# Performance work log

Hardware: AMD Instinct MI355X
Metric: run time of the kernel (lower is better)

## Reference

```python
import jax, jax.numpy as jnp
import numpy as np
from jax import lax

B, T, D, H, L = 2048, 512, 64, 16, 10
LOG2PI = float(np.log(2.0 * np.pi))


def _gru_cell(x, h, Wih, Whh, bih, bhh):
    # torch GRUCell gate order: r, z, n
    gi = x @ Wih.T + bih
    gh = h @ Whh.T + bhh
    ir, iz, inn = jnp.split(gi, 3, axis=-1)
    hr, hz, hn = jnp.split(gh, 3, axis=-1)
    r = jax.nn.sigmoid(ir + hr)
    z = jax.nn.sigmoid(iz + hz)
    n = jnp.tanh(inn + r * hn)
    return (1.0 - z) * n + z * h


def _mlp_head(h, W1, b1, W2, b2, Wmu, bmu, Wcov, bcov):
    hh = jax.nn.relu(h @ W1.T + b1)
    hh = jax.nn.relu(hh @ W2.T + b2)
    mu = hh @ Wmu.T + bmu
    sigma = jnp.exp(hh @ Wcov.T + bcov)
    return mu, sigma


def setup_inputs():
    key = jax.random.key(0)
    ks = jax.random.split(key, 24)

    def he(k, shape, fan_in):
        return jax.random.normal(k, shape, dtype=jnp.float32) * np.float32(np.sqrt(2.0 / fan_in))

    z = lambda *s: jnp.zeros(s, jnp.float32)
    p = {}
    p['x'] = jax.random.normal(ks[0], (B, T, D), dtype=jnp.float32)
    p['eps'] = jax.random.normal(ks[1], (B, T, L), dtype=jnp.float32)
    # bidirectional inference GRU
    p['bi_Wih_f'] = he(ks[2], (3 * H, D), D); p['bi_Whh_f'] = he(ks[3], (3 * H, H), H)
    p['bi_bih_f'] = z(3 * H); p['bi_bhh_f'] = z(3 * H)
    p['bi_Wih_b'] = he(ks[4], (3 * H, D), D); p['bi_Whh_b'] = he(ks[5], (3 * H, H), H)
    p['bi_bih_b'] = z(3 * H); p['bi_bhh_b'] = z(3 * H)
    # inference GRUCell on [z_prev, context]
    p['infz_Wih'] = he(ks[6], (3 * H, L + 2 * H), L + 2 * H); p['infz_Whh'] = he(ks[7], (3 * H, H), H)
    p['infz_bih'] = z(3 * H); p['infz_bhh'] = z(3 * H)
    # inference MLP
    p['inf_W1'] = he(ks[8], (H, H), H); p['inf_b1'] = z(H)
    p['inf_W2'] = he(ks[9], (H, H), H); p['inf_b2'] = z(H)
    p['inf_Wmu'] = he(ks[10], (L, H), H); p['inf_bmu'] = z(L)
    p['inf_Wcov'] = he(ks[11], (L, H), H); p['inf_bcov'] = z(L)
    # generative prior GRUCell + MLP (frozen in torch)
    p['genz_Wih'] = he(ks[12], (3 * H, L), L); p['genz_Whh'] = he(ks[13], (3 * H, H), H)
    p['genz_bih'] = z(3 * H); p['genz_bhh'] = z(3 * H)
    p['genzmlp_W1'] = he(ks[14], (H, H), H); p['genzmlp_b1'] = z(H)
    p['genzmlp_W2'] = he(ks[15], (H, H), H); p['genzmlp_b2'] = z(H)
    p['genzmlp_Wmu'] = he(ks[16], (L, H), H); p['genzmlp_bmu'] = z(L)
    p['genzmlp_Wcov'] = he(ks[17], (L, H), H); p['genzmlp_bcov'] = z(L)
    # generative emission GRUCell + MLP (outputs 3*D)
    p['genr_Wih'] = he(ks[18], (3 * H, L), L); p['genr_Whh'] = he(ks[19], (3 * H, H), H)
    p['genr_bih'] = z(3 * H); p['genr_bhh'] = z(3 * H)
    p['genr_W1'] = he(ks[20], (H, H), H); p['genr_b1'] = z(H)
    p['genr_W2'] = he(ks[21], (3 * D, H), H); p['genr_b2'] = z(3 * D)
    return p


def _forward(x, eps, bi_Wih_f, bi_Whh_f, bi_bih_f, bi_bhh_f, bi_Wih_b, bi_Whh_b, bi_bih_b, bi_bhh_b,
             infz_Wih, infz_Whh, infz_bih, infz_bhh,
             inf_W1, inf_b1, inf_W2, inf_b2, inf_Wmu, inf_bmu, inf_Wcov, inf_bcov,
             genz_Wih, genz_Whh, genz_bih, genz_bhh,
             genzmlp_W1, genzmlp_b1, genzmlp_W2, genzmlp_b2, genzmlp_Wmu, genzmlp_bmu, genzmlp_Wcov, genzmlp_bcov,
             genr_Wih, genr_Whh, genr_bih, genr_bhh, genr_W1, genr_b1, genr_W2, genr_b2):
    b, t, d = x.shape
    xt = jnp.transpose(x, (1, 0, 2))      # [T, B, D] time-major
    eps_t = jnp.transpose(eps, (1, 0, 2))  # [T, B, L]
    h0 = jnp.zeros((b, H), x.dtype)

    def fstep(h, xin):
        h2 = _gru_cell(xin, h, bi_Wih_f, bi_Whh_f, bi_bih_f, bi_bhh_f)
        return h2, h2

    def bstep(h, xin):
        h2 = _gru_cell(xin, h, bi_Wih_b, bi_Whh_b, bi_bih_b, bi_bhh_b)
        return h2, h2

    _, fwd = lax.scan(fstep, h0, xt)               # [T, B, H]
    _, bwd_rev = lax.scan(bstep, h0, xt[::-1])
    bwd = bwd_rev[::-1]                            # [T, B, H]

    pad = jnp.zeros((1, b, H), x.dtype)
    h_right = jnp.concatenate([pad, fwd[:-1]], axis=0)   # h^{->}_{t-1}
    h_left = jnp.concatenate([bwd[1:], pad], axis=0)     # h^{<-}_{t+1}
    ctx = jnp.concatenate([h_right, h_left], axis=-1)    # [T, B, 2H]

    def step(carry, inp):
        h_z, h_gz, h_gr, z_prev = carry
        c, e, xi = inp
        h_z = _gru_cell(jnp.concatenate([z_prev, c], axis=-1), h_z, infz_Wih, infz_Whh, infz_bih, infz_bhh)
        q_mu, q_sig = _mlp_head(h_z, inf_W1, inf_b1, inf_W2, inf_b2, inf_Wmu, inf_bmu, inf_Wcov, inf_bcov)
        h_gz = _gru_cell(z_prev, h_gz, genz_Wih, genz_Whh, genz_bih, genz_bhh)
        p_mu, p_sig = _mlp_head(h_gz, genzmlp_W1, genzmlp_b1, genzmlp_W2, genzmlp_b2, genzmlp_Wmu, genzmlp_bmu, genzmlp_Wcov, genzmlp_bcov)
        # KL(N(q_mu,q_sig) || N(p_mu,p_sig))
        kl = jnp.log(p_sig / q_sig) + (q_sig * q_sig + (q_mu - p_mu) ** 2) / (2.0 * p_sig * p_sig) - 0.5
        kl_t = kl.sum(axis=-1).mean()
        z_t = q_mu + q_sig * e  # rsample
        h_gr = _gru_cell(z_t, h_gr, genr_Wih, genr_Whh, genr_bih, genr_bhh)
        r = jax.nn.relu(h_gr @ genr_W1.T + genr_b1) @ genr_W2.T + genr_b2  # [B, 3D]
        r_mu = r[:, :d]
        r_diag = jnp.exp(r[:, d:2 * d]) + 1e-4
        w = r[:, 2 * d:]  # rank-1 cov factor
        # LowRankMVN log_prob via Woodbury (rank 1): Cov = D + w w^T
        delta = xi - r_mu
        dinv = 1.0 / r_diag
        wd = w * dinv
        cap = 1.0 + jnp.sum(wd * w, axis=-1)  # capacitance
        maha = jnp.sum(delta * delta * dinv, axis=-1) - jnp.sum(wd * delta, axis=-1) ** 2 / cap
        logdet = jnp.sum(jnp.log(r_diag), axis=-1) + jnp.log(cap)
        logp = -0.5 * (d * LOG2PI + logdet + maha)
        nll_t = -logp.mean()
        return (h_z, h_gz, h_gr, z_t), (kl_t, nll_t)

    z0 = jnp.zeros((b, L), x.dtype)
    carry0 = (h0, h0, h0, z0)
    _, (kls, nlls) = lax.scan(step, carry0, (ctx, eps_t, xt))
    return nlls.sum(), kls.sum()


def reference(x, eps, bi_Wih_f, bi_Whh_f, bi_bih_f, bi_bhh_f, bi_Wih_b, bi_Whh_b, bi_bih_b, bi_bhh_b,
              infz_Wih, infz_Whh, infz_bih, infz_bhh,
              inf_W1, inf_b1, inf_W2, inf_b2, inf_Wmu, inf_bmu, inf_Wcov, inf_bcov,
              genz_Wih, genz_Whh, genz_bih, genz_bhh,
              genzmlp_W1, genzmlp_b1, genzmlp_W2, genzmlp_b2, genzmlp_Wmu, genzmlp_bmu, genzmlp_Wcov, genzmlp_bcov,
              genr_Wih, genr_Whh, genr_bih, genr_bhh, genr_W1, genr_b1, genr_W2, genr_b2):
    return _forward(x, eps, bi_Wih_f, bi_Whh_f, bi_bih_f, bi_bhh_f, bi_Wih_b, bi_Whh_b, bi_bih_b, bi_bhh_b,
                    infz_Wih, infz_Whh, infz_bih, infz_bhh,
                    inf_W1, inf_b1, inf_W2, inf_b2, inf_Wmu, inf_bmu, inf_Wcov, inf_bcov,
                    genz_Wih, genz_Whh, genz_bih, genz_bhh,
                    genzmlp_W1, genzmlp_b1, genzmlp_W2, genzmlp_b2, genzmlp_Wmu, genzmlp_bmu, genzmlp_Wcov, genzmlp_bcov,
                    genr_Wih, genr_Whh, genr_bih, genr_bhh, genr_W1, genr_b1, genr_W2, genr_b2)
```

## Files before the change

kernel.cpp:

```cpp
#include <hip/hip_runtime.h>

namespace {

typedef __attribute__((ext_vector_type(4))) _Float16 half4v;
typedef __attribute__((ext_vector_type(4))) float   float4v;
typedef unsigned int u32;

#define MFMA16(a,b,c) __builtin_amdgcn_mfma_f32_16x16x16f16((a),(b),(c),0,0,0)

constexpr int Bb = 2048;
constexpr int Tt = 512;
constexpr float LOG2PI_ = 1.8378770664093453f;

struct InPtrs { const float* p[42]; };

__device__ __forceinline__ float rcpf(float x){ return __builtin_amdgcn_rcpf(x); }
__device__ __forceinline__ float sigm(float x){ return rcpf(1.0f + __expf(-x)); }
__device__ __forceinline__ float tanh_(float x){ return 1.0f - 2.0f*rcpf(1.0f + __expf(2.0f*x)); }

__device__ __forceinline__ void barrier_lds(){
  asm volatile("s_waitcnt lgkmcnt(0)" ::: "memory");
  __builtin_amdgcn_s_barrier();
  asm volatile("" ::: "memory");
}

__global__ void zero2(float* out){ if (threadIdx.x < 2) out[threadIdx.x] = 0.f; }

__device__ __forceinline__ void gru_update(const float4v& Dr, const float4v& Dz,
                                           const float4v& Dn, const float4v& Dh, half4v& hB){
  #pragma unroll
  for (int i = 0; i < 4; ++i){
    const float rr = sigm(Dr[i]);
    const float zz = sigm(Dz[i]);
    const float nn = tanh_(Dn[i] + rr*Dh[i]);
    const float hp = (float)hB[i];
    hB[i] = (_Float16)(nn + zz*(hp - nn));
  }
}

__device__ __forceinline__ half4v relu_pack(const float4v& D){
  half4v o;
  #pragma unroll
  for (int i = 0; i < 4; ++i) o[i] = (_Float16)fmaxf(D[i], 0.f);
  return o;
}

constexpr int CH = 8;
constexpr int NCH = Tt / CH;

__global__ __launch_bounds__(128,1) void bigru(InPtrs ip, _Float16* __restrict__ hf,
                                               _Float16* __restrict__ hb)
{
  const int tid = threadIdx.x;
  const int w = tid >> 6;
  const int l = tid & 63, r = l & 15, q = l >> 4;
  const int dir = blockIdx.y;
  const int base = blockIdx.x * 16;

  const float* __restrict__ x   = ip.p[0];
  const float* __restrict__ Wih = dir ? ip.p[6] : ip.p[2];
  const float* __restrict__ Whh = dir ? ip.p[7] : ip.p[3];
  const float* __restrict__ bih = dir ? ip.p[8] : ip.p[4];
  const float* __restrict__ bhh = dir ? ip.p[9] : ip.p[5];
  _Float16* __restrict__ hout = dir ? hb : hf;

  __shared__ __align__(16) float giS[2][CH][64][12];

  half4v Wi[3][4];
  float  b0[4], b1[4], b2[4];
  float4v xp[CH][4];
  half4v Wh[3];
  float  bh2[4];
  half4v hB = {0,0,0,0};
  const float* xrow = x + (size_t)(base + r) * Tt * 64;

  if (w == 1){
    #pragma unroll
    for (int rt = 0; rt < 3; ++rt)
      #pragma unroll
      for (int kt = 0; kt < 4; ++kt)
        #pragma unroll
        for (int j = 0; j < 4; ++j)
          Wi[rt][kt][j] = (_Float16)Wih[(rt*16 + r)*64 + kt*16 + q*4 + j];
    #pragma unroll
    for (int i = 0; i < 4; ++i){
      const int row = q*4 + i;
      b0[i] = bih[row]      + bhh[row];
      b1[i] = bih[16 + row] + bhh[16 + row];
      b2[i] = bih[32 + row];
    }
    #pragma unroll
    for (int s = 0; s < CH; ++s){
      const int tn = dir ? Tt-1-s : s;
      #pragma unroll
      for (int kt = 0; kt < 4; ++kt)
        xp[s][kt] = *(const float4v*)(xrow + (size_t)tn*64 + kt*16 + q*4);
    }
  } else {
    #pragma unroll
    for (int rt = 0; rt < 3; ++rt)
      #pragma unroll
      for (int j = 0; j < 4; ++j)
        Wh[rt][j] = (_Float16)Whh[(rt*16 + r)*16 + q*4 + j];
    #pragma unroll
    for (int i = 0; i < 4; ++i) bh2[i] = bhh[32 + q*4 + i];
  }

  for (int c = 0; c < NCH; ++c){
    if (w == 1){
      #pragma unroll
      for (int st = 0; st < CH; ++st){
        const int tg = c*CH + st;
        half4v xB[4];
        #pragma unroll
        for (int kt = 0; kt < 4; ++kt)
          #pragma unroll
          for (int j = 0; j < 4; ++j) xB[kt][j] = (_Float16)xp[st][kt][j];
        const int tp = tg + CH;
        if (tp < Tt){
          const int tn = dir ? Tt-1-tp : tp;
          #pragma unroll
          for (int kt = 0; kt < 4; ++kt)
            xp[st][kt] = *(const float4v*)(xrow + (size_t)tn*64 + kt*16 + q*4);
        }
        float4v A0 = {b0[0],b0[1],b0[2],b0[3]};
        float4v A1 = {b1[0],b1[1],b1[2],b1[3]};
        float4v A2 = {b2[0],b2[1],b2[2],b2[3]};
        #pragma unroll
        for (int kt = 0; kt < 4; ++kt){
          A0 = MFMA16(Wi[0][kt], xB[kt], A0);
          A1 = MFMA16(Wi[1][kt], xB[kt], A1);
          A2 = MFMA16(Wi[2][kt], xB[kt], A2);
        }
        float* o = &giS[c&1][st][l][0];
        *(float4v*)(o + 0) = A0;
        *(float4v*)(o + 4) = A1;
        *(float4v*)(o + 8) = A2;
      }
    }
    barrier_lds();
    if (w == 0){
      #pragma unroll
      for (int st = 0; st < CH; ++st){
        const int tg = c*CH + st;
        const int t = dir ? Tt-1-tg : tg;
        const float* gi = &giS[c&1][st][l][0];
        float4v A0 = *(const float4v*)(gi + 0);
        float4v A1 = *(const float4v*)(gi + 4);
        float4v A2 = *(const float4v*)(gi + 8);
        float4v Dh = {bh2[0],bh2[1],bh2[2],bh2[3]};
        A0 = MFMA16(Wh[0], hB, A0);
        A1 = MFMA16(Wh[1], hB, A1);
        Dh = MFMA16(Wh[2], hB, Dh);
        gru_update(A0, A1, A2, Dh, hB);
        *(half4v*)(hout + (((size_t)t*Bb + base + r) << 4) + q*4) = hB;
      }
    }
  }
}

__global__ __launch_bounds__(192,1) void vae_seq(InPtrs ip, const _Float16* __restrict__ hf,
                                                 const _Float16* __restrict__ hb,
                                                 _Float16* __restrict__ hz,
                                                 _Float16* __restrict__ hgz,
                                                 _Float16* __restrict__ hgr)
{
  const int tid = threadIdx.x;
  const int w = tid / 64;
  const int l = tid & 63, r = l & 15, q = l >> 4;
  const int base = blockIdx.x * 16;
  const int row0 = q*4;

  __shared__ u32 zS[3][2][64];
  for (int i = tid; i < 3*2*64; i += 192) ((u32*)zS)[i] = 0u;
  barrier_lds();

  half4v WizA[3][3], WhzA[3], I1A, I2A, IMuA, ICovA;
  float bz0[4], bz1[4], bzn[4], bzh[4], bI1v[4], bI2v[4], bIMu[4], bICov[4];
  half4v hzB = {0,0,0,0}, zB = {0,0,0,0};
  half4v hrR[4], hlR[4];
  float4v eR[4];
  half4v WgzA[3], WhgzA[3];
  float bg0[4], bg1[4], bgn[4], bgh[4];
  half4v hgzB = {0,0,0,0};
  half4v WgrA[3], WhgrA[3];
  float br0[4], br1[4], brn[4], brh[4];
  half4v hgrB = {0,0,0,0};

  const float* erow = ip.p[1] + (size_t)(base + r) * Tt * 10;

  if (w == 0){
    #pragma unroll
    for (int rt = 0; rt < 3; ++rt)
      #pragma unroll
      for (int kt = 0; kt < 3; ++kt)
        #pragma unroll
        for (int j = 0; j < 4; ++j){
          const int k = kt*16 + q*4 + j;
          int c;
          if (kt == 0) c = (k < 10) ? k : -1;
          else if (kt == 1) c = 10 + (k - 16);
          else c = 26 + (k - 32);
          WizA[rt][kt][j] = (c >= 0) ? (_Float16)ip.p[10][(rt*16 + r)*42 + c] : (_Float16)0.f;
        }
    #pragma unroll
    for (int rt = 0; rt < 3; ++rt)
      #pragma unroll
      for (int j = 0; j < 4; ++j)
        WhzA[rt][j] = (_Float16)ip.p[11][(rt*16 + r)*16 + q*4 + j];
    #pragma unroll
    for (int j = 0; j < 4; ++j){
      const int k = q*4 + j;
      I1A[j]  = (_Float16)ip.p[14][r*16 + k];
      I2A[j]  = (_Float16)ip.p[16][r*16 + k];
      IMuA[j] = (r < 10) ? (_Float16)ip.p[18][r*16 + k] : (_Float16)0.f;
      ICovA[j]= (r < 10) ? (_Float16)ip.p[20][r*16 + k] : (_Float16)0.f;
    }
    #pragma unroll
    for (int i = 0; i < 4; ++i){
      const int row = row0 + i;
      bz0[i] = ip.p[12][row]    + ip.p[13][row];
      bz1[i] = ip.p[12][16+row] + ip.p[13][16+row];
      bzn[i] = ip.p[12][32+row];
      bzh[i] = ip.p[13][32+row];
      bI1v[i] = ip.p[15][row];  bI2v[i] = ip.p[17][row];
      bIMu[i]  = (row < 10) ? ip.p[19][row] : 0.f;
      bICov[i] = (row < 10) ? ip.p[21][row] : 0.f;
    }
    #pragma unroll
    for (int s = 0; s < 4; ++s){
      if (s >= 1) hrR[s] = *(const half4v*)(hf + (((size_t)(s-1)*Bb + base + r) << 4) + q*4);
      else { half4v z0 = {0,0,0,0}; hrR[s] = z0; }
      hlR[s] = *(const half4v*)(hb + (((size_t)(s+1)*Bb + base + r) << 4) + q*4);
      float4v et;
      #pragma unroll
      for (int ii = 0; ii < 4; ++ii) et[ii] = (row0 + ii < 10) ? erow[s*10 + row0 + ii] : 0.f;
      eR[s] = et;
    }
  } else if (w == 1){
    #pragma unroll
    for (int rt = 0; rt < 3; ++rt)
      #pragma unroll
      for (int j = 0; j < 4; ++j){
        const int k = q*4 + j;
        WgzA[rt][j]  = (k < 10) ? (_Float16)ip.p[22][(rt*16 + r)*10 + k] : (_Float16)0.f;
        WhgzA[rt][j] = (_Float16)ip.p[23][(rt*16 + r)*16 + k];
      }
    #pragma unroll
    for (int i = 0; i < 4; ++i){
      const int row = row0 + i;
      bg0[i] = ip.p[24][row]    + ip.p[25][row];
      bg1[i] = ip.p[24][16+row] + ip.p[25][16+row];
      bgn[i] = ip.p[24][32+row];
      bgh[i] = ip.p[25][32+row];
    }
  } else {
    #pragma unroll
    for (int rt = 0; rt < 3; ++rt)
      #pragma unroll
      for (int j = 0; j < 4; ++j){
        const int k = q*4 + j;
        WgrA[rt][j]  = (k < 10) ? (_Float16)ip.p[34][(rt*16 + r)*10 + k] : (_Float16)0.f;
        WhgrA[rt][j] = (_Float16)ip.p[35][(rt*16 + r)*16 + k];
      }
    #pragma unroll
    for (int i = 0; i < 4; ++i){
      const int row = row0 + i;
      br0[i] = ip.p[36][row]    + ip.p[37][row];
      br1[i] = ip.p[36][16+row] + ip.p[37][16+row];
      brn[i] = ip.p[36][32+row];
      brh[i] = ip.p[37][32+row];
    }
  }

  for (int ib = 0; ib < Tt + 4; ib += 4){
    #pragma unroll
    for (int k = 0; k < 4; ++k){
      const int i = ib + k;
      if (w == 0){
        if (i < Tt){
          const half4v hrB = hrR[k], hlB = hlR[k];
          const float4v ev = eR[k];
          const int f = i + 4;
          if (f < Tt){
            hrR[k] = *(const half4v*)(hf + (((size_t)(f-1)*Bb + base + r) << 4) + q*4);
            if (f <= Tt-2) hlR[k] = *(const half4v*)(hb + (((size_t)(f+1)*Bb + base + r) << 4) + q*4);
            else { half4v z0 = {0,0,0,0}; hlR[k] = z0; }
            float4v et;
            #pragma unroll
            for (int ii = 0; ii < 4; ++ii) et[ii] = (row0 + ii < 10) ? erow[f*10 + row0 + ii] : 0.f;
            eR[k] = et;
          }
          float4v Dr = {bz0[0],bz0[1],bz0[2],bz0[3]};
          float4v Dz = {bz1[0],bz1[1],bz1[2],bz1[3]};
          float4v Dn = {bzn[0],bzn[1],bzn[2],bzn[3]};
          float4v Dh = {bzh[0],bzh[1],bzh[2],bzh[3]};
          Dr = MFMA16(WizA[0][1], hrB, Dr); Dr = MFMA16(WizA[0][2], hlB, Dr);
          Dz = MFMA16(WizA[1][1], hrB, Dz); Dz = MFMA16(WizA[1][2], hlB, Dz);
          Dn = MFMA16(WizA[2][1], hrB, Dn); Dn = MFMA16(WizA[2][2], hlB, Dn);
          Dr = MFMA16(WhzA[0], hzB, Dr);
          Dz = MFMA16(WhzA[1], hzB, Dz);
          Dh = MFMA16(WhzA[2], hzB, Dh);
          Dr = MFMA16(WizA[0][0], zB, Dr);
          Dz = MFMA16(WizA[1][0], zB, Dz);
          Dn = MFMA16(WizA[2][0], zB, Dn);
          gru_update(Dr, Dz, Dn, Dh, hzB);
          *(half4v*)(hz + (((size_t)i*Bb + base + r) << 4) + q*4) = hzB;

          float4v H1 = {bI1v[0],bI1v[1],bI1v[2],bI1v[3]};
          H1 = MFMA16(I1A, hzB, H1);
          const half4v h1B = relu_pack(H1);
          float4v H2 = {bI2v[0],bI2v[1],bI2v[2],bI2v[3]};
          H2 = MFMA16(I2A, h1B, H2);
          const half4v h2B = relu_pack(H2);
          float4v Qmu  = {bIMu[0],bIMu[1],bIMu[2],bIMu[3]};
          float4v Qpre = {bICov[0],bICov[1],bICov[2],bICov[3]};
          Qmu  = MFMA16(IMuA,  h2B, Qmu);
          Qpre = MFMA16(ICovA, h2B, Qpre);

          const int slot = i % 3;
          #pragma unroll
          for (int ii = 0; ii < 4; ++ii){
            const float qs = __expf(Qpre[ii]);
            zB[ii] = (_Float16)(Qmu[ii] + qs*ev[ii]);
          }
          union { half4v h; u32 u[2]; } zc; zc.h = zB;
          zS[slot][0][l] = zc.u[0];
          zS[slot][1][l] = zc.u[1];
        }
      } else if (w == 1){
        if (i >= 1 && i <= Tt){
          const int s = i - 1;
          const int sp = (s - 1 + 3) % 3;
          union { half4v h; u32 u[2]; } zc;
          zc.u[0] = zS[sp][0][l]; zc.u[1] = zS[sp][1][l];
          const half4v zPrev = zc.h;

          float4v Er = {bg0[0],bg0[1],bg0[2],bg0[3]};
          float4v Ez = {bg1[0],bg1[1],bg1[2],bg1[3]};
          float4v En = {bgn[0],bgn[1],bgn[2],bgn[3]};
          float4v Eh = {bgh[0],bgh[1],bgh[2],bgh[3]};
          Er = MFMA16(WgzA[0], zPrev, Er); Er = MFMA16(WhgzA[0], hgzB, Er);
          Ez = MFMA16(WgzA[1], zPrev, Ez); Ez = MFMA16(WhgzA[1], hgzB, Ez);
          En = MFMA16(WgzA[2], zPrev, En);
          Eh = MFMA16(WhgzA[2], hgzB, Eh);
          gru_update(Er, Ez, En, Eh, hgzB);
          *(half4v*)(hgz + (((size_t)s*Bb + base + r) << 4) + q*4) = hgzB;
        }
      } else {
        if (i >= 2 && i < Tt + 2){
          const int u = i - 2;
          union { half4v h; u32 uu[2]; } zc;
          zc.uu[0] = zS[u % 3][0][l]; zc.uu[1] = zS[u % 3][1][l];
          const half4v zU = zc.h;

          float4v Fr = {br0[0],br0[1],br0[2],br0[3]};
          float4v Fz = {br1[0],br1[1],br1[2],br1[3]};
          float4v Fn = {brn[0],brn[1],brn[2],brn[3]};
          float4v Fh = {brh[0],brh[1],brh[2],brh[3]};
          Fr = MFMA16(WgrA[0], zU, Fr); Fr = MFMA16(WhgrA[0], hgrB, Fr);
          Fz = MFMA16(WgrA[1], zU, Fz); Fz = MFMA16(WhgrA[1], hgrB, Fz);
          Fn = MFMA16(WgrA[2], zU, Fn);
          Fh = MFMA16(WhgrA[2], hgrB, Fh);
          gru_update(Fr, Fz, Fn, Fh, hgrB);
          *(half4v*)(hgr + (((size_t)u*Bb + base + r) << 4) + q*4) = hgrB;
        }
      }
      barrier_lds();
    }
  }
}

__global__ __launch_bounds__(256,2) void epi(InPtrs ip, const _Float16* __restrict__ hz,
                                             const _Float16* __restrict__ hgz,
                                             const _Float16* __restrict__ hgr,
                                             float* __restrict__ out)
{
  const int tid = threadIdx.x;
  const int l = tid & 63, r = l & 15, q = l >> 4;
  const int row0 = q*4;

  if (blockIdx.x < 1024){
    const int wid = blockIdx.x * 4 + (tid >> 6);
    const int u0 = wid * 16;

    half4v I1A, I2A, IMuA, ICovA, Z1A, Z2A, ZMuA, ZCovA;
    float bI1v[4], bI2v[4], bIMu[4], bICov[4], bZ1v[4], bZ2v[4], bZMu[4], bZCov[4];
    #pragma unroll
    for (int j = 0; j < 4; ++j){
      const int k = q*4 + j;
      I1A[j]  = (_Float16)ip.p[14][r*16 + k];
      I2A[j]  = (_Float16)ip.p[16][r*16 + k];
      IMuA[j] = (r < 10) ? (_Float16)ip.p[18][r*16 + k] : (_Float16)0.f;
      ICovA[j]= (r < 10) ? (_Float16)ip.p[20][r*16 + k] : (_Float16)0.f;
      Z1A[j]  = (_Float16)ip.p[26][r*16 + k];
      Z2A[j]  = (_Float16)ip.p[28][r*16 + k];
      ZMuA[j] = (r < 10) ? (_Float16)ip.p[30][r*16 + k] : (_Float16)0.f;
      ZCovA[j]= (r < 10) ? (_Float16)ip.p[32][r*16 + k] : (_Float16)0.f;
    }
    #pragma unroll
    for (int i = 0; i < 4; ++i){
      const int row = row0 + i;
      bI1v[i] = ip.p[15][row];  bI2v[i] = ip.p[17][row];
      bIMu[i]  = (row < 10) ? ip.p[19][row] : 0.f;
      bICov[i] = (row < 10) ? ip.p[21][row] : 0.f;
      bZ1v[i] = ip.p[27][row];  bZ2v[i] = ip.p[29][row];
      bZMu[i]  = (row < 10) ? ip.p[31][row] : 0.f;
      bZCov[i] = (row < 10) ? ip.p[33][row] : 0.f;
    }

    float kl_acc = 0.f;
    for (int k = 0; k < 16; ++k){
      const int u = u0 + k;
      const int tile = u >> 9, t = u & 511;
      const size_t off = (((size_t)t*Bb + tile*16 + r) << 4) + q*4;
      const half4v hzB  = *(const half4v*)(hz  + off);
      const half4v hgzB = *(const half4v*)(hgz + off);

      float4v H1 = {bI1v[0],bI1v[1],bI1v[2],bI1v[3]};
      H1 = MFMA16(I1A, hzB, H1);
      const half4v h1B = relu_pack(H1);
      float4v H2 = {bI2v[0],bI2v[1],bI2v[2],bI2v[3]};
      H2 = MFMA16(I2A, h1B, H2);
      const half4v h2B = relu_pack(H2);
      float4v Qmu  = {bIMu[0],bIMu[1],bIMu[2],bIMu[3]};
      float4v Qpre = {bICov[0],bICov[1],bICov[2],bICov[3]};
      Qmu  = MFMA16(IMuA,  h2B, Qmu);
      Qpre = MFMA16(ICovA, h2B, Qpre);

      float4v G1 = {bZ1v[0],bZ1v[1],bZ1v[2],bZ1v[3]};
      G1 = MFMA16(Z1A, hgzB, G1);
      const half4v g1B = relu_pack(G1);
      float4v G2 = {bZ2v[0],bZ2v[1],bZ2v[2],bZ2v[3]};
      G2 = MFMA16(Z2A, g1B, G2);
      const half4v g2B = relu_pack(G2);
      float4v Pmu  = {bZMu[0],bZMu[1],bZMu[2],bZMu[3]};
      float4v Ppre = {bZCov[0],bZCov[1],bZCov[2],bZCov[3]};
      Pmu  = MFMA16(ZMuA,  g2B, Pmu);
      Ppre = MFMA16(ZCovA, g2B, Ppre);

      #pragma unroll
      for (int ii = 0; ii < 4; ++ii){
        const float qs = __expf(Qpre[ii]);
        const float dm = Qmu[ii] - Pmu[ii];
        kl_acc += (Ppre[ii] - Qpre[ii]) + (qs*qs + dm*dm)*0.5f*__expf(-2.f*Ppre[ii]) - 0.5f;
      }
    }
    #pragma unroll
    for (int m = 1; m < 64; m <<= 1) kl_acc += __shfl_xor(kl_acc, m, 64);
    if (l == 0) atomicAdd(&out[1], kl_acc * (1.f/(float)Bb));
  } else {
    const int wid = (blockIdx.x - 1024) * 4 + (tid >> 6);
    const int u0 = wid * 16;

    half4v R1A, R2A[12];
    float bR1v[4], bR2v[12][4];
    #pragma unroll
    for (int j = 0; j < 4; ++j){
      const int k = q*4 + j;
      R1A[j] = (_Float16)ip.p[38][r*16 + k];
      #pragma unroll
      for (int m = 0; m < 12; ++m)
        R2A[m][j] = (_Float16)ip.p[40][(m*16 + r)*16 + k];
    }
    #pragma unroll
    for (int i = 0; i < 4; ++i){
      const int row = row0 + i;
      bR1v[i] = ip.p[39][row];
      #pragma unroll
      for (int m = 0; m < 12; ++m) bR2v[m][i] = ip.p[41][m*16 + row];
    }

    float nll_acc = 0.f;
    for (int k = 0; k < 16; ++k){
      const int u = u0 + k;
      const int tile = u >> 9, t = u & 511;
      const half4v hgrB = *(const half4v*)(hgr + (((size_t)t*Bb + tile*16 + r) << 4) + q*4);
      const float* xrow = ip.p[0] + ((size_t)(tile*16 + r) * Tt + t) * 64;
      float4v xv[4];
      #pragma unroll
      for (int m = 0; m < 4; ++m) xv[m] = *(const float4v*)(xrow + m*16 + q*4);

      float4v R1D = {bR1v[0],bR1v[1],bR1v[2],bR1v[3]};
      R1D = MFMA16(R1A, hgrB, R1D);
      const half4v r1B = relu_pack(R1D);

      float s1 = 0.f, s2 = 0.f, s3 = 0.f, s4 = 0.f;
      #pragma unroll
      for (int m = 0; m < 4; ++m){
        float4v Dmu = {bR2v[m][0],bR2v[m][1],bR2v[m][2],bR2v[m][3]};
        float4v Ddp = {bR2v[4+m][0],bR2v[4+m][1],bR2v[4+m][2],bR2v[4+m][3]};
        float4v Dw  = {bR2v[8+m][0],bR2v[8+m][1],bR2v[8+m][2],bR2v[8+m][3]};
        Dmu = MFMA16(R2A[m],   r1B, Dmu);
        Ddp = MFMA16(R2A[4+m], r1B, Ddp);
        Dw  = MFMA16(R2A[8+m], r1B, Dw);
        #pragma unroll
        for (int ii = 0; ii < 4; ++ii){
          const float diag = __expf(Ddp[ii]) + 1e-4f;
          const float dinv = rcpf(diag);
          const float delta = xv[m][ii] - Dmu[ii];
          const float wv = Dw[ii];
          s1 += delta*delta*dinv;
          s2 += wv*wv*dinv;
          s3 += wv*dinv*delta;
          s4 += __logf(diag);
        }
      }
      s1 += __shfl_xor(s1, 16, 64); s1 += __shfl_xor(s1, 32, 64);
      s2 += __shfl_xor(s2, 16, 64); s2 += __shfl_xor(s2, 32, 64);
      s3 += __shfl_xor(s3, 16, 64); s3 += __shfl_xor(s3, 32, 64);
      s4 += __shfl_xor(s4, 16, 64); s4 += __shfl_xor(s4, 32, 64);
      const float cap = 1.f + s2;
      const float maha = s1 - s3*s3*rcpf(cap);
      const float logdet = s4 + __logf(cap);
      nll_acc += 0.5f*(64.f*LOG2PI_ + logdet + maha);
    }
    #pragma unroll
    for (int m = 1; m < 64; m <<= 1) nll_acc += __shfl_xor(nll_acc, m, 64);
    if (l == 0) atomicAdd(&out[0], nll_acc * 0.25f * (1.f/(float)Bb));
  }
}

}

extern "C" void kernel_launch(void* const* d_in, const int* in_sizes, int n_in,
                              void* d_out, int out_size, void* d_ws, size_t ws_size,
                              hipStream_t stream)
{
  InPtrs ip;
  for (int i = 0; i < 42; ++i) ip.p[i] = (const float*)d_in[i];
  float* out = (float*)d_out;

  const size_t SZ = (size_t)Tt * Bb * 16;
  _Float16* hf  = (_Float16*)d_ws;
  _Float16* hb  = hf  + SZ;
  _Float16* hz  = hb  + SZ;
  _Float16* hgz = hz  + SZ;
  _Float16* hgr = hgz + SZ;

  zero2<<<1, 64, 0, stream>>>(out);
  dim3 gb(Bb/16, 2);
  bigru<<<gb, 128, 0, stream>>>(ip, hf, hb);
  vae_seq<<<Bb/16, 192, 0, stream>>>(ip, hf, hb, hz, hgz, hgr);
  epi<<<2048, 256, 0, stream>>>(ip, hz, hgz, hgr, out);
}
```

Before: 1.029 ms.

## Split input projection across two warps, halve barriers, widen epilogue grid, fold zeroing

The bidirectional GRU now uses two producer waves that each compute input-gate projections for alternating timesteps, which halves per-wave work and prefetch registers. The zeroing of the outputs moves into the bigru kernel, removing one launch. In the sequential VAE kernel the z ring buffer grows from 3 to 8 slots, the pipeline stage offsets are widened, and the block barrier fires only every other step. The epilogue launches twice as many blocks with half the work per wave. The barrier skipping depends on the deeper ring and the larger lag being sufficient to avoid races, and zeroing inside bigru assumes it happens before any epilogue atomics, which stream ordering provides.

Measured after the change: 1.135 ms. 1.1x slower.

```diff
diff --git a/kernel.cpp b/kernel.cpp
--- a/kernel.cpp
+++ b/kernel.cpp
@@ -23,8 +23,6 @@
   __builtin_amdgcn_s_barrier();
   asm volatile("" ::: "memory");
 }
-
-__global__ void zero2(float* out){ if (threadIdx.x < 2) out[threadIdx.x] = 0.f; }
 
 __device__ __forceinline__ void gru_update(const float4v& Dr, const float4v& Dz,
                                            const float4v& Dn, const float4v& Dh, half4v& hB){
@@ -48,14 +46,16 @@
 constexpr int CH = 8;
 constexpr int NCH = Tt / CH;
 
-__global__ __launch_bounds__(128,1) void bigru(InPtrs ip, _Float16* __restrict__ hf,
-                                               _Float16* __restrict__ hb)
+__global__ __launch_bounds__(192,1) void bigru(InPtrs ip, _Float16* __restrict__ hf,
+                                               _Float16* __restrict__ hb, float* __restrict__ out)
 {
   const int tid = threadIdx.x;
-  const int w = tid >> 6;
+  const int w = tid / 64;
   const int l = tid & 63, r = l & 15, q = l >> 4;
   const int dir = blockIdx.y;
   const int base = blockIdx.x * 16;
+
+  if (blockIdx.x == 0 && blockIdx.y == 0 && tid < 2) out[tid] = 0.f;
 
   const float* __restrict__ x   = ip.p[0];
   const float* __restrict__ Wih = dir ? ip.p[6] : ip.p[2];
@@ -68,13 +68,14 @@
 
   half4v Wi[3][4];
   float  b0[4], b1[4], b2[4];
-  float4v xp[CH][4];
+  float4v xp[4][4];
   half4v Wh[3];
   float  bh2[4];
   half4v hB = {0,0,0,0};
   const float* xrow = x + (size_t)(base + r) * Tt * 64;
-
-  if (w == 1){
+  const int p = w - 1;
+
+  if (w >= 1){
     #pragma unroll
     for (int rt = 0; rt < 3; ++rt)
       #pragma unroll
@@ -90,11 +91,12 @@
       b2[i] = bih[32 + row];
     }
     #pragma unroll
-    for (int s = 0; s < CH; ++s){
-      const int tn = dir ? Tt-1-s : s;
+    for (int sl = 0; sl < 4; ++sl){
+      const int tg = sl*2 + p;
+      const int tn = dir ? Tt-1-tg : tg;
       #pragma unroll
       for (int kt = 0; kt < 4; ++kt)
-        xp[s][kt] = *(const float4v*)(xrow + (size_t)tn*64 + kt*16 + q*4);
+        xp[sl][kt] = *(const float4v*)(xrow + (size_t)tn*64 + kt*16 + q*4);
     }
   } else {
     #pragma unroll
@@ -107,21 +109,22 @@
   }
 
   for (int c = 0; c < NCH; ++c){
-    if (w == 1){
-      #pragma unroll
-      for (int st = 0; st < CH; ++st){
+    if (w >= 1){
+      #pragma unroll
+      for (int sl = 0; sl < 4; ++sl){
+        const int st = sl*2 + p;
         const int tg = c*CH + st;
         half4v xB[4];
         #pragma unroll
         for (int kt = 0; kt < 4; ++kt)
           #pragma unroll
-          for (int j = 0; j < 4; ++j) xB[kt][j] = (_Float16)xp[st][kt][j];
+          for (int j = 0; j < 4; ++j) xB[kt][j] = (_Float16)xp[sl][kt][j];
         const int tp = tg + CH;
         if (tp < Tt){
           const int tn = dir ? Tt-1-tp : tp;
           #pragma unroll
           for (int kt = 0; kt < 4; ++kt)
-            xp[st][kt] = *(const float4v*)(xrow + (size_t)tn*64 + kt*16 + q*4);
+            xp[sl][kt] = *(const float4v*)(xrow + (size_t)tn*64 + kt*16 + q*4);
         }
         float4v A0 = {b0[0],b0[1],b0[2],b0[3]};
         float4v A1 = {b1[0],b1[1],b1[2],b1[3]};
@@ -171,8 +174,8 @@
   const int base = blockIdx.x * 16;
   const int row0 = q*4;
 
-  __shared__ u32 zS[3][2][64];
-  for (int i = tid; i < 3*2*64; i += 192) ((u32*)zS)[i] = 0u;
+  __shared__ u32 zS[8][2][64];
+  for (int i = tid; i < 8*2*64; i += 192) ((u32*)zS)[i] = 0u;
   barrier_lds();
 
   half4v WizA[3][3], WhzA[3], I1A, I2A, IMuA, ICovA;
@@ -318,21 +321,21 @@
           Qmu  = MFMA16(IMuA,  h2B, Qmu);
           Qpre = MFMA16(ICovA, h2B, Qpre);
 
-          const int slot = i % 3;
           #pragma unroll
           for (int ii = 0; ii < 4; ++ii){
             const float qs = __expf(Qpre[ii]);
             zB[ii] = (_Float16)(Qmu[ii] + qs*ev[ii]);
           }
           union { half4v h; u32 u[2]; } zc; zc.h = zB;
+          const int slot = i & 7;
           zS[slot][0][l] = zc.u[0];
           zS[slot][1][l] = zc.u[1];
         }
       } else if (w == 1){
-        if (i >= 1 && i <= Tt){
-          const int s = i - 1;
-          const int sp = (s - 1 + 3) % 3;
+        if (i >= 2 && i < Tt + 2){
+          const int s = i - 2;
           union { half4v h; u32 u[2]; } zc;
+          const int sp = (s - 1) & 7;
           zc.u[0] = zS[sp][0][l]; zc.u[1] = zS[sp][1][l];
           const half4v zPrev = zc.h;
 
@@ -348,10 +351,11 @@
           *(half4v*)(hgz + (((size_t)s*Bb + base + r) << 4) + q*4) = hgzB;
         }
       } else {
-        if (i >= 2 && i < Tt + 2){
-          const int u = i - 2;
+        if (i >= 4 && i < Tt + 4){
+          const int u = i - 4;
           union { half4v h; u32 uu[2]; } zc;
-          zc.uu[0] = zS[u % 3][0][l]; zc.uu[1] = zS[u % 3][1][l];
+          const int su = u & 7;
+          zc.uu[0] = zS[su][0][l]; zc.uu[1] = zS[su][1][l];
           const half4v zU = zc.h;
 
           float4v Fr = {br0[0],br0[1],br0[2],br0[3]};
@@ -366,7 +370,7 @@
           *(half4v*)(hgr + (((size_t)u*Bb + base + r) << 4) + q*4) = hgrB;
         }
       }
-      barrier_lds();
+      if (k & 1) barrier_lds();
     }
   }
 }
@@ -380,9 +384,9 @@
   const int l = tid & 63, r = l & 15, q = l >> 4;
   const int row0 = q*4;
 
-  if (blockIdx.x < 1024){
+  if (blockIdx.x < 2048){
     const int wid = blockIdx.x * 4 + (tid >> 6);
-    const int u0 = wid * 16;
+    const int u0 = wid * 8;
 
     half4v I1A, I2A, IMuA, ICovA, Z1A, Z2A, ZMuA, ZCovA;
     float bI1v[4], bI2v[4], bIMu[4], bICov[4], bZ1v[4], bZ2v[4], bZMu[4], bZCov[4];
@@ -410,7 +414,7 @@
     }
 
     float kl_acc = 0.f;
-    for (int k = 0; k < 16; ++k){
+    for (int k = 0; k < 8; ++k){
       const int u = u0 + k;
       const int tile = u >> 9, t = u & 511;
       const size_t off = (((size_t)t*Bb + tile*16 + r) << 4) + q*4;
@@ -450,8 +454,8 @@
     for (int m = 1; m < 64; m <<= 1) kl_acc += __shfl_xor(kl_acc, m, 64);
     if (l == 0) atomicAdd(&out[1], kl_acc * (1.f/(float)Bb));
   } else {
-    const int wid = (blockIdx.x - 1024) * 4 + (tid >> 6);
-    const int u0 = wid * 16;
+    const int wid = (blockIdx.x - 2048) * 4 + (tid >> 6);
+    const int u0 = wid * 8;
 
     half4v R1A, R2A[12];
     float bR1v[4], bR2v[12][4];
@@ -472,7 +476,7 @@
     }
 
     float nll_acc = 0.f;
-    for (int k = 0; k < 16; ++k){
+    for (int k = 0; k < 8; ++k){
       const int u = u0 + k;
       const int tile = u >> 9, t = u & 511;
       const half4v hgrB = *(const half4v*)(hgr + (((size_t)t*Bb + tile*16 + r) << 4) + q*4);
@@ -538,9 +542,8 @@
   _Float16* hgz = hz  + SZ;
   _Float16* hgr = hgz + SZ;
 
-  zero2<<<1, 64, 0, stream>>>(out);
   dim3 gb(Bb/16, 2);
-  bigru<<<gb, 128, 0, stream>>>(ip, hf, hb);
+  bigru<<<gb, 192, 0, stream>>>(ip, hf, hb, out);
   vae_seq<<<Bb/16, 192, 0, stream>>>(ip, hf, hb, hz, hgz, hgr);
-  epi<<<2048, 256, 0, stream>>>(ip, hz, hgz, hgr, out);
-}
+  epi<<<4096, 256, 0, stream>>>(ip, hz, hgz, hgr, out);
+}
```
